# Kernel optimization log

Hardware: AMD Instinct MI355X
Metric: run time of the kernel (lower is better)

## Reference

```python
import jax, jax.numpy as jnp
import numpy as np

ACT_GUARD = 2.0   # 2 ** act_guard_bit (act_guard_bit = 1)
WGT_GUARD = 2.0   # 2 ** weight_guard_bit (weight_guard_bit = 1)


def _ste_round(v):
    # straight-through estimator round (QNMethod.STE)
    return v + jax.lax.stop_gradient(jnp.round(v) - v)


def setup_inputs() -> dict:
    key = jax.random.key(0)
    k_x, k_w, k_b = jax.random.split(key, 3)
    B, S, DIN, DOUT = 4, 2048, 2048, 8192
    ACT_INIT_S, ACT_INIT_Q, LOG_S_INIT = -10.0, 10.0, -8.0
    x = jax.random.normal(k_x, (B, S, DIN), dtype=jnp.float32)
    weight = jax.random.normal(k_w, (DOUT, DIN), dtype=jnp.float32) * 0.02
    bias = jax.random.normal(k_b, (DOUT,), dtype=jnp.float32) * 0.01
    log_act_s = jnp.full((1,), ACT_INIT_S, dtype=jnp.float32)
    log_act_q = jnp.full((1,), ACT_INIT_Q, dtype=jnp.float32)
    act_b = jnp.full((1,), -jnp.exp2(ACT_INIT_Q - 1.0), dtype=jnp.float32)  # -512
    log_wght_s = jnp.full((DOUT, 1), LOG_S_INIT, dtype=jnp.float32)
    return {"x": x, "weight": weight, "bias": bias, "log_act_s": log_act_s,
            "log_act_q": log_act_q, "act_b": act_b, "log_wght_s": log_wght_s}


def reference(x, weight, bias, log_act_s, log_act_q, act_b, log_wght_s):
    # --- activation fake-quant (per-tensor) ---
    s = jnp.exp2(log_act_s)                       # [1]
    q = jnp.exp2(log_act_q)                       # [1]
    zp = jnp.round(act_b / s * ACT_GUARD) / ACT_GUARD * s  # guard-bit rounded zero point
    lo, hi = zp, zp + q - s
    qx = _ste_round((jnp.clip(x, lo, hi) - zp) / s)
    x_dq = qx * s + zp                            # dequantized activations

    # --- weight fake-quant (per-channel over out dim, amin/amax over dim 1) ---
    w_scale = jnp.exp2(log_wght_s)                # [DOUT, 1]
    wmin = jnp.min(weight, axis=1, keepdims=True)
    wmax = jnp.max(weight, axis=1, keepdims=True)
    qwmin = jnp.round(wmin / w_scale * WGT_GUARD) / WGT_GUARD * w_scale
    qwmax = jnp.round(wmax / w_scale * WGT_GUARD) / WGT_GUARD * w_scale
    qw = _ste_round((jnp.clip(weight, qwmin, qwmax) - qwmin) / w_scale)
    w_dq = qw * w_scale + qwmin                   # dequantized weights

    # --- affine: y = x @ W.T + b ---
    return jnp.einsum('bsi,oi->bso', x_dq, w_dq) + bias
```

## Files before the change

### kernel.cpp

```cpp
#include <hip/hip_runtime.h>
#include <hip/hip_bf16.h>


using f16x8 = __attribute__((ext_vector_type(8))) _Float16;
using f32x4 = __attribute__((ext_vector_type(4))) float;

#define AS1 __attribute__((address_space(1)))
#define AS3 __attribute__((address_space(3)))

static __device__ __forceinline__ void gload_lds16(const void* g, void* l) {
    __builtin_amdgcn_global_load_lds((const AS1 void*)g, (AS3 void*)l, 16, 0, 0);
}

__global__ __launch_bounds__(256) void wquant_kernel(
    const float* __restrict__ W, const float* __restrict__ lws,
    _Float16* __restrict__ Wq) {
    constexpr int K = 2048;
    const int row = blockIdx.x;
    const int t = threadIdx.x;
    const float* w = W + (size_t)row * K;

    float4 v0 = ((const float4*)w)[t * 2];
    float4 v1 = ((const float4*)w)[t * 2 + 1];
    float vals[8] = {v0.x, v0.y, v0.z, v0.w, v1.x, v1.y, v1.z, v1.w};

    float mn = vals[0], mx = vals[0];
#pragma unroll
    for (int i = 1; i < 8; ++i) {
        mn = fminf(mn, vals[i]);
        mx = fmaxf(mx, vals[i]);
    }
#pragma unroll
    for (int off = 32; off >= 1; off >>= 1) {
        mn = fminf(mn, __shfl_xor(mn, off));
        mx = fmaxf(mx, __shfl_xor(mx, off));
    }
    __shared__ float smn[4], smx[4];
    if ((t & 63) == 0) { smn[t >> 6] = mn; smx[t >> 6] = mx; }
    __syncthreads();
    mn = fminf(fminf(smn[0], smn[1]), fminf(smn[2], smn[3]));
    mx = fmaxf(fmaxf(smx[0], smx[1]), fmaxf(smx[2], smx[3]));

    const float l = lws[row];
    const float ws = exp2f(l);
    const float rs = exp2f(-l);
    const float qwmin = rintf(mn * rs * 2.0f) * 0.5f * ws;
    const float qwmax = rintf(mx * rs * 2.0f) * 0.5f * ws;

    f16x8 out;
#pragma unroll
    for (int i = 0; i < 8; ++i) {
        float c = fminf(fmaxf(vals[i], qwmin), qwmax);
        float qw = rintf((c - qwmin) * rs);
        out[i] = (_Float16)(qw * ws + qwmin);
    }
    *(f16x8*)&Wq[(size_t)row * K + (size_t)t * 8] = out;
}

__global__ __launch_bounds__(256) void xquant_kernel(
    const float* __restrict__ X,
    const float* __restrict__ las, const float* __restrict__ laq,
    const float* __restrict__ ab, _Float16* __restrict__ Xq) {
    const float ls = las[0], lq = laq[0];
    const float s = exp2f(ls);
    const float rs = exp2f(-ls);
    const float q = exp2f(lq);
    const float zp = rintf(ab[0] * rs * 2.0f) * 0.5f * s;
    const float lo = zp;
    const float hi = (zp + q) - s;

    const size_t base = ((size_t)blockIdx.x * 256 + threadIdx.x) * 8;
    float4 v0 = *(const float4*)&X[base];
    float4 v1 = *(const float4*)&X[base + 4];
    float vals[8] = {v0.x, v0.y, v0.z, v0.w, v1.x, v1.y, v1.z, v1.w};

    f16x8 out;
#pragma unroll
    for (int i = 0; i < 8; ++i) {
        float c = fminf(fmaxf(vals[i], lo), hi);
        float qx = rintf((c - zp) * rs);
        out[i] = (_Float16)(qx * s + zp);
    }
    *(f16x8*)&Xq[base] = out;
}

__global__ __launch_bounds__(512, 2) void gemm_kernel(
    const _Float16* __restrict__ A, const _Float16* __restrict__ B,
    const float* __restrict__ bias, float* __restrict__ C) {
    constexpr int N = 8192, K = 2048;
    constexpr int KT = K / 64;
    constexpr int NBN = N / 256;

    __shared__ char smem[131072];

    const int bid = blockIdx.x;
    const int cpx = gridDim.x >> 3;
    const int swzb = (bid & 7) * cpx + (bid >> 3);
    const int bm = swzb / NBN;
    const int bn = swzb % NBN;

    const int t = threadIdx.x;
    const int lane = t & 63;
    const int wid = t >> 6;
    const int wr = wid >> 2;
    const int wc = wid & 3;
    const int l15 = lane & 15;
    const int lq = lane >> 4;

    const int d0 = t * 16, d1 = d0 + 8192;
    const int r0 = d0 >> 7, c0 = (((d0 & 127) ^ (((d0 >> 7) & 7) << 4)) >> 1);
    const int r1 = d1 >> 7, c1 = (((d1 & 127) ^ (((d1 >> 7) & 7) << 4)) >> 1);
    const _Float16* Agb = A + (size_t)bm * 256 * K;
    const _Float16* Bgb = B + (size_t)bn * 256 * K;

    const int cp0 = (lq * 16) ^ ((l15 & 7) << 4);
    const int cp1 = cp0 ^ 64;

    f32x4 acc[8][4] = {};
    f16x8 fA0[4][2], fA1[4][2], fB0[2][2], fB1[2][2];

#define STAGE(GB, RO, DBS, H, KS) do {                                         \
        const _Float16* _g = (GB) + (size_t)((H) * 128) * K + (size_t)(KS) * 64;\
        char* _l = smem + (RO) + ((DBS) * 2 + (H)) * 16384;                    \
        gload_lds16(_g + (size_t)r0 * K + c0, _l + d0);                        \
        gload_lds16(_g + (size_t)r1 * K + c1, _l + d1);                        \
    } while (0)

#define LDAF(dst, DBv, MLO) do {                                               \
        const char* _s = smem + ((DBv) * 2 + wr) * 16384 + l15 * 128;          \
        _Pragma("unroll")                                                      \
        for (int _m = 0; _m < 4; ++_m) {                                       \
            dst[_m][0] = *(const f16x8*)(_s + ((MLO) + _m) * 2048 + cp0);      \
            dst[_m][1] = *(const f16x8*)(_s + ((MLO) + _m) * 2048 + cp1);      \
        }                                                                      \
    } while (0)

#define LDBF(dst, DBv, NLO) do {                                               \
        const char* _s = smem + 65536 + ((DBv) * 2 + (wc >> 1)) * 16384 +      \
                         (wc & 1) * 8192 + l15 * 128;                          \
        _Pragma("unroll")                                                      \
        for (int _n = 0; _n < 2; ++_n) {                                       \
            dst[_n][0] = *(const f16x8*)(_s + ((NLO) + _n) * 2048 + cp0);      \
            dst[_n][1] = *(const f16x8*)(_s + ((NLO) + _n) * 2048 + cp1);      \
        }                                                                      \
    } while (0)

#define QMFMA(MLO, NLO, AF, BF) do {                                           \
        _Pragma("unroll")                                                      \
        for (int _m = 0; _m < 4; ++_m)                                         \
            _Pragma("unroll")                                                  \
            for (int _n = 0; _n < 2; ++_n) {                                   \
                f32x4 _c = acc[(MLO) + _m][(NLO) + _n];                        \
                _c = __builtin_amdgcn_mfma_f32_16x16x32_f16(                   \
                    AF[_m][0], BF[_n][0], _c, 0, 0, 0);                        \
                _c = __builtin_amdgcn_mfma_f32_16x16x32_f16(                   \
                    AF[_m][1], BF[_n][1], _c, 0, 0, 0);                        \
                acc[(MLO) + _m][(NLO) + _n] = _c;                              \
            }                                                                  \
    } while (0)

#define HALFITER(DBv, S1, S2, S3, S4, VMW) do {                                \
                                                          \
        LDAF(fA0, DBv, 0); LDBF(fB0, DBv, 0);                                  \
        S1;                                                                    \
        asm volatile("s_waitcnt lgkmcnt(8)" ::: "memory");                     \
        __builtin_amdgcn_s_barrier();                                          \
        asm volatile("s_waitcnt lgkmcnt(0)" ::: "memory");                     \
        __builtin_amdgcn_s_setprio(1);                                         \
        QMFMA(0, 0, fA0, fB0);                                                 \
        __builtin_amdgcn_s_setprio(0);                                         \
        __builtin_amdgcn_s_barrier();                                          \
                                                           \
        LDBF(fB1, DBv, 2);                                                     \
        S2;                                                                    \
        __builtin_amdgcn_s_barrier();                                          \
        asm volatile("s_waitcnt lgkmcnt(0)" ::: "memory");                     \
        __builtin_amdgcn_s_setprio(1);                                         \
        QMFMA(0, 2, fA0, fB1);                                                 \
        __builtin_amdgcn_s_setprio(0);                                         \
        __builtin_amdgcn_s_barrier();                                          \
                                                           \
        LDAF(fA1, DBv, 4);                                                     \
        S3;                                                                    \
        __builtin_amdgcn_s_barrier();                                          \
        asm volatile("s_waitcnt lgkmcnt(0)" ::: "memory");                     \
        __builtin_amdgcn_s_setprio(1);                                         \
        QMFMA(4, 2, fA1, fB1);                                                 \
        __builtin_amdgcn_s_setprio(0);                                         \
        __builtin_amdgcn_s_barrier();                                          \
                                                           \
        S4;                                                                    \
        __builtin_amdgcn_s_barrier();                                          \
        __builtin_amdgcn_s_setprio(1);                                         \
        QMFMA(4, 0, fA1, fB0);                                                 \
        __builtin_amdgcn_s_setprio(0);                                         \
        asm volatile("s_waitcnt vmcnt(" #VMW ")" ::: "memory");                \
        __builtin_amdgcn_s_barrier();                                          \
    } while (0)

    STAGE(Bgb, 65536, 0, 0, 0);
    STAGE(Agb, 0,     0, 0, 0);
    STAGE(Agb, 0,     0, 1, 0);
    STAGE(Bgb, 65536, 0, 1, 0);
    STAGE(Bgb, 65536, 1, 0, 1);
    STAGE(Bgb, 65536, 1, 1, 1);
    asm volatile("s_waitcnt vmcnt(4)" ::: "memory");
    __builtin_amdgcn_s_barrier();

    for (int it = 0; it < KT / 2; ++it) {
        const int b  = 2 * it + 1;
        const int aN = (2 * it + 2 < KT) ? 2 * it + 2 : KT - 2;
        const int bN = (2 * it + 3 < KT) ? 2 * it + 3 : KT - 1;

        HALFITER(0,
                 STAGE(Agb, 0,     1, 0, b),
                 STAGE(Agb, 0,     1, 1, b),
                 STAGE(Bgb, 65536, 0, 0, aN),
                 STAGE(Agb, 0,     0, 0, aN), 4);
        HALFITER(1,
                 STAGE(Agb, 0,     0, 1, aN),
                 STAGE(Bgb, 65536, 0, 1, aN),
                 STAGE(Bgb, 65536, 1, 0, bN),
                 STAGE(Bgb, 65536, 1, 1, bN), 4);
    }
#undef HALFITER
#undef QMFMA
#undef LDBF
#undef LDAF
#undef STAGE

#pragma unroll
    for (int m = 0; m < 8; ++m) {
        const int row = bm * 256 + wr * 128 + m * 16 + lq * 4;
#pragma unroll
        for (int n = 0; n < 4; ++n) {
            const int col = bn * 256 + wc * 64 + n * 16 + l15;
            const float bv = bias[col];
#pragma unroll
            for (int r = 0; r < 4; ++r) {
                C[(size_t)(row + r) * N + col] = acc[m][n][r] + bv;
            }
        }
    }
}

extern "C" void kernel_launch(void* const* d_in, const int* in_sizes, int n_in,
                              void* d_out, int out_size, void* d_ws, size_t ws_size,
                              hipStream_t stream) {
    const float* x    = (const float*)d_in[0];
    const float* w    = (const float*)d_in[1];
    const float* bias = (const float*)d_in[2];
    const float* las  = (const float*)d_in[3];
    const float* laq  = (const float*)d_in[4];
    const float* ab   = (const float*)d_in[5];
    const float* lws  = (const float*)d_in[6];
    float* out = (float*)d_out;

    constexpr size_t MK = (size_t)8192 * 2048;
    _Float16* xq = (_Float16*)d_ws;
    _Float16* wq = (_Float16*)((char*)d_ws + MK * sizeof(_Float16));

    xquant_kernel<<<8192, 256, 0, stream>>>(x, las, laq, ab, xq);
    wquant_kernel<<<8192, 256, 0, stream>>>(w, lws, wq);
    gemm_kernel<<<1024, 512, 0, stream>>>(xq, wq, bias, out);
}
```

Baseline: 290.3 us.

## Software-pipeline LDS fragment loads across MFMA phases in GEMM main loop

Restructures the K-loop so the LDS fragment loads for the next phase are issued before the current phase's MFMAs. Waits now use partial lgkmcnt counts with sched_barrier instead of fully draining before each MFMA block. The fA0/fB0 loads for the next half-iteration are prefetched at the tail of the current one, and the number of barriers per half-iteration drops. This is meant to hide LDS read latency behind matrix math, at the cost of tighter dependency ordering and correctness risk around buffer reuse.

```diff
diff --git a/kernel.cpp b/kernel.cpp
--- a/kernel.cpp
+++ b/kernel.cpp
@@ -159,44 +159,13 @@
             }                                                                  \
     } while (0)
 
-#define HALFITER(DBv, S1, S2, S3, S4, VMW) do {                                \
-                                                          \
-        LDAF(fA0, DBv, 0); LDBF(fB0, DBv, 0);                                  \
-        S1;                                                                    \
-        asm volatile("s_waitcnt lgkmcnt(8)" ::: "memory");                     \
-        __builtin_amdgcn_s_barrier();                                          \
-        asm volatile("s_waitcnt lgkmcnt(0)" ::: "memory");                     \
-        __builtin_amdgcn_s_setprio(1);                                         \
-        QMFMA(0, 0, fA0, fB0);                                                 \
-        __builtin_amdgcn_s_setprio(0);                                         \
-        __builtin_amdgcn_s_barrier();                                          \
-                                                           \
-        LDBF(fB1, DBv, 2);                                                     \
-        S2;                                                                    \
-        __builtin_amdgcn_s_barrier();                                          \
-        asm volatile("s_waitcnt lgkmcnt(0)" ::: "memory");                     \
-        __builtin_amdgcn_s_setprio(1);                                         \
-        QMFMA(0, 2, fA0, fB1);                                                 \
-        __builtin_amdgcn_s_setprio(0);                                         \
-        __builtin_amdgcn_s_barrier();                                          \
-                                                           \
-        LDAF(fA1, DBv, 4);                                                     \
-        S3;                                                                    \
-        __builtin_amdgcn_s_barrier();                                          \
-        asm volatile("s_waitcnt lgkmcnt(0)" ::: "memory");                     \
-        __builtin_amdgcn_s_setprio(1);                                         \
-        QMFMA(4, 2, fA1, fB1);                                                 \
-        __builtin_amdgcn_s_setprio(0);                                         \
-        __builtin_amdgcn_s_barrier();                                          \
-                                                           \
-        S4;                                                                    \
-        __builtin_amdgcn_s_barrier();                                          \
-        __builtin_amdgcn_s_setprio(1);                                         \
-        QMFMA(4, 0, fA1, fB0);                                                 \
-        __builtin_amdgcn_s_setprio(0);                                         \
-        asm volatile("s_waitcnt vmcnt(" #VMW ")" ::: "memory");                \
-        __builtin_amdgcn_s_barrier();                                          \
-    } while (0)
+#define LGKM(NN) do {                                                          \
+        asm volatile("s_waitcnt lgkmcnt(" #NN ")" ::: "memory");               \
+        __builtin_amdgcn_sched_barrier(0);                                     \
+    } while (0)
+#define VMC(NN) asm volatile("s_waitcnt vmcnt(" #NN ")" ::: "memory")
+#define BAR()   __builtin_amdgcn_s_barrier()
+#define PRIO(P) __builtin_amdgcn_s_setprio(P)
 
     STAGE(Bgb, 65536, 0, 0, 0);
     STAGE(Agb, 0,     0, 0, 0);
@@ -204,30 +173,68 @@
     STAGE(Bgb, 65536, 0, 1, 0);
     STAGE(Bgb, 65536, 1, 0, 1);
     STAGE(Bgb, 65536, 1, 1, 1);
-    asm volatile("s_waitcnt vmcnt(4)" ::: "memory");
-    __builtin_amdgcn_s_barrier();
+    VMC(4);
+    BAR();
+    LDAF(fA0, 0, 0);
+    LDBF(fB0, 0, 0);
 
     for (int it = 0; it < KT / 2; ++it) {
         const int b  = 2 * it + 1;
         const int aN = (2 * it + 2 < KT) ? 2 * it + 2 : KT - 2;
         const int bN = (2 * it + 3 < KT) ? 2 * it + 3 : KT - 1;
 
-        HALFITER(0,
-                 STAGE(Agb, 0,     1, 0, b),
-                 STAGE(Agb, 0,     1, 1, b),
-                 STAGE(Bgb, 65536, 0, 0, aN),
-                 STAGE(Agb, 0,     0, 0, aN), 4);
-        HALFITER(1,
-                 STAGE(Agb, 0,     0, 1, aN),
-                 STAGE(Bgb, 65536, 0, 1, aN),
-                 STAGE(Bgb, 65536, 1, 0, bN),
-                 STAGE(Bgb, 65536, 1, 1, bN), 4);
-    }
-#undef HALFITER
+        BAR();
+        LDBF(fB1, 0, 2);
+        STAGE(Agb, 0, 1, 0, b);
+        LGKM(4);
+        PRIO(1); QMFMA(0, 0, fA0, fB0); PRIO(0);
+        BAR();
+        LDAF(fA1, 0, 4);
+        STAGE(Agb, 0, 1, 1, b);
+        LGKM(8);
+        PRIO(1); QMFMA(0, 2, fA0, fB1); PRIO(0);
+        BAR();
+        STAGE(Bgb, 65536, 0, 0, aN);
+        LGKM(0);
+        PRIO(1); QMFMA(4, 2, fA1, fB1); PRIO(0);
+        VMC(2);
+        BAR();
+        LDAF(fA0, 1, 0);
+        STAGE(Agb, 0, 0, 0, aN);
+        LGKM(8);
+        PRIO(1); QMFMA(4, 0, fA1, fB0); PRIO(0);
+        LDBF(fB0, 1, 0);
+
+        BAR();
+        LDBF(fB1, 1, 2);
+        STAGE(Agb, 0, 0, 1, aN);
+        LGKM(4);
+        PRIO(1); QMFMA(0, 0, fA0, fB0); PRIO(0);
+        BAR();
+        LDAF(fA1, 1, 4);
+        STAGE(Bgb, 65536, 0, 1, aN);
+        LGKM(8);
+        PRIO(1); QMFMA(0, 2, fA0, fB1); PRIO(0);
+        BAR();
+        STAGE(Bgb, 65536, 1, 0, bN);
+        LGKM(0);
+        PRIO(1); QMFMA(4, 2, fA1, fB1); PRIO(0);
+        VMC(2);
+        BAR();
+        LDAF(fA0, 0, 0);
+        STAGE(Bgb, 65536, 1, 1, bN);
+        LGKM(8);
+        PRIO(1); QMFMA(4, 0, fA1, fB0); PRIO(0);
+        LDBF(fB0, 0, 0);
+    }
+#undef STAGE
+#undef LDAF
+#undef LDBF
 #undef QMFMA
-#undef LDBF
-#undef LDAF
-#undef STAGE
+#undef LGKM
+#undef VMC
+#undef BAR
+#undef PRIO
 
 #pragma unroll
     for (int m = 0; m < 8; ++m) {
```

Result: slower. 318.3 us (+9.6%).
